# Kernel optimization log

Measured on AMD Instinct MI355X. Metric: run time of the kernel, lower is better.

## Reference

```python
import jax, jax.numpy as jnp
import numpy as np

B, N, F, D, DB, C = 1024, 200000, 32, 128, 256, 96


def _ln(x, g, b, eps=1e-5):
    m = x.mean(-1, keepdims=True)
    v = ((x - m) ** 2).mean(-1, keepdims=True)
    return (x - m) / jnp.sqrt(v + eps) * g + b


def setup_inputs() -> dict:
    key = jax.random.key(0)
    ks = jax.random.split(key, 24)
    s = 0.05
    inp = {
        'x_num': jax.random.normal(ks[0], (B, F), jnp.float32),
        'cand_x_num': jax.random.normal(ks[1], (N, F), jnp.float32),
        'cand_y': jax.random.normal(ks[2], (N,), jnp.float32),
        'W_in': jax.random.normal(ks[3], (F, D), jnp.float32) * s,
        'b_in': jnp.zeros((D,), jnp.float32),
        'enc_w1': jax.random.normal(ks[4], (D, DB), jnp.float32) * s,
        'enc_b1': jnp.zeros((DB,), jnp.float32),
        'enc_w2': jax.random.normal(ks[5], (DB, D), jnp.float32) * s,
        'enc_b2': jnp.zeros((D,), jnp.float32),
        'ln_mix_g': jnp.ones((D,), jnp.float32),
        'ln_mix_b': jnp.zeros((D,), jnp.float32),
        'K_w': jax.random.normal(ks[6], (D, D), jnp.float32) * s,
        'K_b': jnp.zeros((D,), jnp.float32),
        'lab_w': jax.random.normal(ks[7], (1, D), jnp.float32) * s,
        'lab_b': jnp.zeros((D,), jnp.float32),
        'T_w1': jax.random.normal(ks[8], (D, DB), jnp.float32) * s,
        'T_b1': jnp.zeros((DB,), jnp.float32),
        'T_w2': jax.random.normal(ks[9], (DB, D), jnp.float32) * s,  # no bias
        'pred_ln_g': jnp.ones((D,), jnp.float32),
        'pred_ln_b': jnp.zeros((D,), jnp.float32),
        'pred_w1': jax.random.normal(ks[10], (D, DB), jnp.float32) * s,
        'pred_b1': jnp.zeros((DB,), jnp.float32),
        'pred_w2': jax.random.normal(ks[11], (DB, D), jnp.float32) * s,
        'pred_b2': jnp.zeros((D,), jnp.float32),
        'head_ln_g': jnp.ones((D,), jnp.float32),
        'head_ln_b': jnp.zeros((D,), jnp.float32),
        'head_w': jax.random.normal(ks[12], (D, 1), jnp.float32) * s,
        'head_b': jnp.zeros((1,), jnp.float32),
        'context_size': C,
    }
    return inp


def _forward(x_num, cand_x_num, cand_y, W_in, b_in, enc_w1, enc_b1, enc_w2, enc_b2,
             ln_mix_g, ln_mix_b, K_w, K_b, lab_w, lab_b, T_w1, T_b1, T_w2,
             pred_ln_g, pred_ln_b, pred_w1, pred_b1, pred_w2, pred_b2,
             head_ln_g, head_ln_b, head_w, head_b, context_size):
    def enc(z):
        h = z @ W_in + b_in                                   # [*, D]
        h = h + (jax.nn.relu(h @ enc_w1 + enc_b1) @ enc_w2 + enc_b2)
        k = _ln(h, ln_mix_g, ln_mix_b) @ K_w + K_b
        return h, k

    cand_k = enc(cand_x_num)[1]                               # [N, D]
    x, k = enc(x_num)                                         # [B, D]

    # brute-force kNN: negative squared L2 via matmul + square sums
    k2 = (k * k).sum(-1, keepdims=True)                       # [B, 1]
    ck2 = (cand_k * cand_k).sum(-1)                           # [N]
    sims = 2.0 * (k @ cand_k.T) - k2 - ck2[None, :]           # [B, N]
    _, idx = jax.lax.top_k(sims, context_size)                # [B, C]

    context_k = cand_k[idx]                                   # [B, C, D]
    sim_c = 2.0 * jnp.einsum('bd,bcd->bc', k, context_k) - k2 - (context_k ** 2).sum(-1)
    probs = jax.nn.softmax(sim_c, axis=-1)                    # [B, C]

    ctx_y = cand_y[idx][..., None] @ lab_w + lab_b            # [B, C, D]
    diff = k[:, None, :] - context_k                          # [B, C, D]
    vals = ctx_y + jax.nn.relu(diff @ T_w1 + T_b1) @ T_w2     # [B, C, D]
    context_x = jnp.einsum('bc,bcd->bd', probs, vals)         # [B, D]

    x = x + context_x
    h = _ln(x, pred_ln_g, pred_ln_b)
    x = x + (jax.nn.relu(h @ pred_w1 + pred_b1) @ pred_w2 + pred_b2)
    out = jax.nn.relu(_ln(x, head_ln_g, head_ln_b)) @ head_w + head_b
    return out                                                # [B, 1]


def reference(x_num, cand_x_num, cand_y, W_in, b_in, enc_w1, enc_b1, enc_w2, enc_b2,
              ln_mix_g, ln_mix_b, K_w, K_b, lab_w, lab_b, T_w1, T_b1, T_w2,
              pred_ln_g, pred_ln_b, pred_w1, pred_b1, pred_w2, pred_b2,
              head_ln_g, head_ln_b, head_w, head_b, context_size):
    return _forward(x_num, cand_x_num, cand_y, W_in, b_in, enc_w1, enc_b1, enc_w2, enc_b2,
                    ln_mix_g, ln_mix_b, K_w, K_b, lab_w, lab_b, T_w1, T_b1, T_w2,
                    pred_ln_g, pred_ln_b, pred_w1, pred_b1, pred_w2, pred_b2,
                    head_ln_g, head_ln_b, head_w, head_b, context_size)
```

## Files before the change

### kernel.cpp

```cpp
#include <hip/hip_runtime.h>
#include <hip/hip_bf16.h>

#define NC 200000
#define NCP 200064
#define NCT 1563
#define NRG 196
#define CTR 8
#define SCAP2 32
#define CROW (NRG * SCAP2)
#define SREG 25
#define BB 1024
#define DD 128
#define DBH 256
#define CS 96

typedef __attribute__((ext_vector_type(8))) short bf16x8;
typedef __attribute__((ext_vector_type(4))) float f32x4;

#define LDH 136
#define LDU 264

__device__ inline uint4 pack8(const float4 a, const float4 b) {
  union { __hip_bfloat16 h[8]; uint4 v; } r;
  r.h[0] = __float2bfloat16(a.x); r.h[1] = __float2bfloat16(a.y);
  r.h[2] = __float2bfloat16(a.z); r.h[3] = __float2bfloat16(a.w);
  r.h[4] = __float2bfloat16(b.x); r.h[5] = __float2bfloat16(b.y);
  r.h[6] = __float2bfloat16(b.z); r.h[7] = __float2bfloat16(b.w);
  return r.v;
}

__device__ inline unsigned encf(float v) {
  unsigned b = __float_as_uint(v);
  return (b & 0x80000000u) ? ~b : (b | 0x80000000u);
}
__device__ inline float decf(unsigned u) {
  return __uint_as_float((u & 0x80000000u) ? (u ^ 0x80000000u) : ~u);
}
__device__ inline unsigned long long mkkey(float v, int idx) {
  unsigned u = encf(v);
  return (((unsigned long long)(~u)) << 32) | (unsigned)idx;
}

__device__ inline void gload16(const void* g, void* l) {
  __builtin_amdgcn_global_load_lds((const __attribute__((address_space(1))) void*)g,
                                   (__attribute__((address_space(3))) void*)l, 16, 0, 0);
}

__global__ __launch_bounds__(256) void k_prep(const float* __restrict__ w1,
                                              const float* __restrict__ w2,
                                              const float* __restrict__ kw,
                                              const float* __restrict__ tw1,
                                              __hip_bfloat16* __restrict__ w1t,
                                              __hip_bfloat16* __restrict__ w2t,
                                              __hip_bfloat16* __restrict__ kwt,
                                              __hip_bfloat16* __restrict__ tw1t) {
  const int i = blockIdx.x * 256 + threadIdx.x;
  if (i < 32768) {
    const int u = i >> 7, j = i & 127;
    w1t[i] = __float2bfloat16(w1[j * DBH + u]);
    tw1t[i] = __float2bfloat16(tw1[j * DBH + u]);
  }
  if (i < 32768) {
    const int d = i >> 8, u = i & 255;
    w2t[i] = __float2bfloat16(w2[u * DD + d]);
  }
  if (i < 16384) {
    const int d = i >> 7, j = i & 127;
    kwt[i] = __float2bfloat16(kw[j * DD + d]);
  }
}

__global__ __launch_bounds__(256) void k_pad(__hip_bfloat16* __restrict__ ckb16,
                                             float* __restrict__ ck2) {
  const int i = blockIdx.x * 256 + threadIdx.x;
  if (i < (NCP - NC) * DD) ckb16[(size_t)NC * DD + i] = __float2bfloat16(0.f);
  if (i < (NCP - NC)) ck2[NC + i] = 1e9f;
}

__global__ __launch_bounds__(256) void k_e1(const float* __restrict__ X,
                                            const float* __restrict__ W,
                                            const float* __restrict__ bias,
                                            float* __restrict__ H) {
  __shared__ float Xs[32 * 32];
  const int tid = threadIdx.x;
  const int r0 = blockIdx.x * 32;
  ((float4*)Xs)[tid] = ((const float4*)(X + (size_t)r0 * 32))[tid];
  __syncthreads();
  const int d0 = tid & 63;
  const int rh = tid >> 6;
  float acc0[8], acc1[8];
  const float b0 = bias[d0], b1 = bias[d0 + 64];
#pragma unroll
  for (int r = 0; r < 8; ++r) { acc0[r] = b0; acc1[r] = b1; }
#pragma unroll
  for (int k4 = 0; k4 < 8; ++k4) {
    float w0[4], w1[4];
#pragma unroll
    for (int kk = 0; kk < 4; ++kk) {
      w0[kk] = W[(k4 * 4 + kk) * DD + d0];
      w1[kk] = W[(k4 * 4 + kk) * DD + d0 + 64];
    }
#pragma unroll
    for (int r = 0; r < 8; ++r) {
      float4 x4 = ((const float4*)(Xs + (rh * 8 + r) * 32))[k4];
      acc0[r] += x4.x * w0[0] + x4.y * w0[1] + x4.z * w0[2] + x4.w * w0[3];
      acc1[r] += x4.x * w1[0] + x4.y * w1[1] + x4.z * w1[2] + x4.w * w1[3];
    }
  }
#pragma unroll
  for (int r = 0; r < 8; ++r) {
    const size_t row = (size_t)(r0 + rh * 8 + r);
    H[row * DD + d0] = acc0[r];
    H[row * DD + d0 + 64] = acc1[r];
  }
}

__global__ __launch_bounds__(256) void k_e23m(float* __restrict__ H,
                                              const __hip_bfloat16* __restrict__ W1t,
                                              const float* __restrict__ B1,
                                              const __hip_bfloat16* __restrict__ W2t,
                                              const float* __restrict__ B2) {
  __shared__ __hip_bfloat16 Hs[64 * LDH];
  __shared__ __hip_bfloat16 Us[64 * LDU];
  const int tid = threadIdx.x;
  const int r0 = blockIdx.x * 64;
#pragma unroll
  for (int i = 0; i < 4; ++i) {
    const int e8 = i * 256 + tid;
    const int row = e8 >> 4, c8 = e8 & 15;
    const float* src = H + (size_t)(r0 + row) * DD + c8 * 8;
    float4 f0 = *(const float4*)(src);
    float4 f1 = *(const float4*)(src + 4);
    *(uint4*)(Hs + row * LDH + c8 * 8) = pack8(f0, f1);
  }
  __syncthreads();
  const int l = tid & 63, w = tid >> 6;
  const int lr = l & 15, lg = l >> 4;
  {
    f32x4 acc[4][4] = {};
#pragma unroll
    for (int kk = 0; kk < 4; ++kk) {
      bf16x8 a[4], b[4];
#pragma unroll
      for (int mi = 0; mi < 4; ++mi)
        a[mi] = *(const bf16x8*)(Hs + (mi * 16 + lr) * LDH + kk * 32 + lg * 8);
#pragma unroll
      for (int ni = 0; ni < 4; ++ni)
        b[ni] = *(const bf16x8*)(W1t + (size_t)(w * 64 + ni * 16 + lr) * DD + kk * 32 + lg * 8);
#pragma unroll
      for (int mi = 0; mi < 4; ++mi)
#pragma unroll
        for (int ni = 0; ni < 4; ++ni)
          acc[mi][ni] = __builtin_amdgcn_mfma_f32_16x16x32_bf16(a[mi], b[ni], acc[mi][ni], 0, 0, 0);
    }
#pragma unroll
    for (int ni = 0; ni < 4; ++ni) {
      const int col = w * 64 + ni * 16 + lr;
      const float bb = B1[col];
#pragma unroll
      for (int mi = 0; mi < 4; ++mi)
#pragma unroll
        for (int r = 0; r < 4; ++r) {
          const int row = mi * 16 + lg * 4 + r;
          Us[row * LDU + col] = __float2bfloat16(fmaxf(acc[mi][ni][r] + bb, 0.f));
        }
    }
  }
  __syncthreads();
  {
    f32x4 acc[4][2] = {};
#pragma unroll
    for (int kk = 0; kk < 8; ++kk) {
      bf16x8 a[4], b[2];
#pragma unroll
      for (int mi = 0; mi < 4; ++mi)
        a[mi] = *(const bf16x8*)(Us + (mi * 16 + lr) * LDU + kk * 32 + lg * 8);
#pragma unroll
      for (int ni = 0; ni < 2; ++ni)
        b[ni] = *(const bf16x8*)(W2t + (size_t)(w * 32 + ni * 16 + lr) * DBH + kk * 32 + lg * 8);
#pragma unroll
      for (int mi = 0; mi < 4; ++mi)
#pragma unroll
        for (int ni = 0; ni < 2; ++ni)
          acc[mi][ni] = __builtin_amdgcn_mfma_f32_16x16x32_bf16(a[mi], b[ni], acc[mi][ni], 0, 0, 0);
    }
#pragma unroll
    for (int ni = 0; ni < 2; ++ni) {
      const int col = w * 32 + ni * 16 + lr;
      const float bb = B2[col];
#pragma unroll
      for (int mi = 0; mi < 4; ++mi)
#pragma unroll
        for (int r = 0; r < 4; ++r) {
          const int row = mi * 16 + lg * 4 + r;
          const size_t g = (size_t)(r0 + row) * DD + col;
          H[g] = H[g] + acc[mi][ni][r] + bb;
        }
    }
  }
}

__global__ __launch_bounds__(256) void k_e4m(const float* __restrict__ H,
                                             const float* __restrict__ g,
                                             const float* __restrict__ bln,
                                             const __hip_bfloat16* __restrict__ Kwt,
                                             const float* __restrict__ Kb,
                                             float* __restrict__ Kout,
                                             __hip_bfloat16* __restrict__ Kb16,
                                             float* __restrict__ k2out) {
  __shared__ __hip_bfloat16 Ls[64 * LDH];
  __shared__ float k2s[64];
  const int tid = threadIdx.x;
  const int r0 = blockIdx.x * 64;
  if (tid < 64) k2s[tid] = 0.f;
  {
    const int row = tid >> 2, q = tid & 3;
    const float* hr = H + (size_t)(r0 + row) * DD + q * 32;
    float v[32];
#pragma unroll
    for (int i = 0; i < 8; ++i) {
      float4 f = ((const float4*)hr)[i];
      v[i * 4 + 0] = f.x; v[i * 4 + 1] = f.y; v[i * 4 + 2] = f.z; v[i * 4 + 3] = f.w;
    }
    float s = 0.f;
#pragma unroll
    for (int i = 0; i < 32; ++i) s += v[i];
    s += __shfl_xor(s, 1); s += __shfl_xor(s, 2);
    const float mean = s * (1.f / 128.f);
    float vs = 0.f;
#pragma unroll
    for (int i = 0; i < 32; ++i) { float d = v[i] - mean; vs += d * d; }
    vs += __shfl_xor(vs, 1); vs += __shfl_xor(vs, 2);
    const float rstd = 1.f / sqrtf(vs * (1.f / 128.f) + 1e-5f);
#pragma unroll
    for (int i = 0; i < 4; ++i) {
      float t[8];
#pragma unroll
      for (int j = 0; j < 8; ++j) {
        const int col = q * 32 + i * 8 + j;
        t[j] = (v[i * 8 + j] - mean) * rstd * g[col] + bln[col];
      }
      float4 f0 = {t[0], t[1], t[2], t[3]}, f1 = {t[4], t[5], t[6], t[7]};
      *(uint4*)(Ls + row * LDH + q * 32 + i * 8) = pack8(f0, f1);
    }
  }
  __syncthreads();
  const int l = tid & 63, w = tid >> 6;
  const int lr = l & 15, lg = l >> 4;
  f32x4 acc[4][2] = {};
#pragma unroll
  for (int kk = 0; kk < 4; ++kk) {
    bf16x8 a[4], b[2];
#pragma unroll
    for (int mi = 0; mi < 4; ++mi)
      a[mi] = *(const bf16x8*)(Ls + (mi * 16 + lr) * LDH + kk * 32 + lg * 8);
#pragma unroll
    for (int ni = 0; ni < 2; ++ni)
      b[ni] = *(const bf16x8*)(Kwt + (size_t)(w * 32 + ni * 16 + lr) * DD + kk * 32 + lg * 8);
#pragma unroll
    for (int mi = 0; mi < 4; ++mi)
#pragma unroll
      for (int ni = 0; ni < 2; ++ni)
        acc[mi][ni] = __builtin_amdgcn_mfma_f32_16x16x32_bf16(a[mi], b[ni], acc[mi][ni], 0, 0, 0);
  }
  float p[4][4];
#pragma unroll
  for (int mi = 0; mi < 4; ++mi)
#pragma unroll
    for (int r = 0; r < 4; ++r) p[mi][r] = 0.f;
#pragma unroll
  for (int ni = 0; ni < 2; ++ni) {
    const int col = w * 32 + ni * 16 + lr;
    const float kb = Kb[col];
#pragma unroll
    for (int mi = 0; mi < 4; ++mi)
#pragma unroll
      for (int r = 0; r < 4; ++r) {
        const float val = acc[mi][ni][r] + kb;
        const int row = mi * 16 + lg * 4 + r;
        const size_t gg = (size_t)(r0 + row) * DD + col;
        Kout[gg] = val;
        Kb16[gg] = __float2bfloat16(val);
        p[mi][r] += val * val;
      }
  }
#pragma unroll
  for (int mi = 0; mi < 4; ++mi)
#pragma unroll
    for (int r = 0; r < 4; ++r) {
      float t = p[mi][r];
      t += __shfl_xor(t, 1); t += __shfl_xor(t, 2);
      t += __shfl_xor(t, 4); t += __shfl_xor(t, 8);
      if (lr == 0) atomicAdd(&k2s[mi * 16 + lg * 4 + r], t);
    }
  __syncthreads();
  if (tid < 64) k2out[r0 + tid] = k2s[tid];
}

__global__ __launch_bounds__(256) void k_simsA(const __hip_bfloat16* __restrict__ A,
                                               const __hip_bfloat16* __restrict__ Bm,
                                               const float* __restrict__ ck2,
                                               float* __restrict__ rmaxpart) {
  __shared__ __hip_bfloat16 Bs[128 * 128];
  __shared__ float part[2][128];
  const int tid = threadIdx.x;
  const int bid = blockIdx.x;
  const int gq = bid >> 6, rt = (bid >> 3) & 7, xq = bid & 7;
  const int range = gq * 8 + xq;
  if (range >= NRG) return;
  const int m0 = rt * 128;
  const int l = tid & 63, w = tid >> 6;
  const int wm = w >> 1, wn = w & 1;
  const int lr = l & 15, lg = l >> 4;
  bf16x8 a[4][4];
#pragma unroll
  for (int mi = 0; mi < 4; ++mi) {
    const __hip_bfloat16* ar = A + (size_t)(m0 + wm * 64 + mi * 16 + lr) * DD + lg * 8;
#pragma unroll
    for (int kk = 0; kk < 4; ++kk) a[mi][kk] = *(const bf16x8*)(ar + kk * 32);
  }
  float vmax[4][4];
#pragma unroll
  for (int mi = 0; mi < 4; ++mi)
#pragma unroll
    for (int r = 0; r < 4; ++r) vmax[mi][r] = -1e30f;
  for (int i = 0; i < CTR; ++i) {
    const int ct = range * CTR + i;
    if (ct >= NCT) break;
    const int n0 = ct * 128;
    {
      const char* gbase = (const char*)(Bm + (size_t)n0 * DD);
#pragma unroll
      for (int j = 0; j < 8; ++j) {
        const int r = w * 32 + j * 4 + (l >> 4);
        const int b = ((l & 15) * 16) ^ ((r & 7) << 4);
        gload16(gbase + (size_t)r * 256 + b, (char*)Bs + w * 8192 + j * 1024);
      }
    }
    float c2l[4];
#pragma unroll
    for (int ni = 0; ni < 4; ++ni) c2l[ni] = 0.5f * ck2[n0 + wn * 64 + ni * 16 + lr];
    __syncthreads();
    f32x4 acc[4][4] = {};
#pragma unroll
    for (int kk = 0; kk < 4; ++kk) {
      bf16x8 b[4];
#pragma unroll
      for (int ni = 0; ni < 4; ++ni) {
        const int row = wn * 64 + ni * 16 + lr;
        const int boff = (kk * 64 + lg * 16) ^ ((row & 7) << 4);
        b[ni] = *(const bf16x8*)((const char*)Bs + row * 256 + boff);
      }
#pragma unroll
      for (int mi = 0; mi < 4; ++mi)
#pragma unroll
        for (int ni = 0; ni < 4; ++ni)
          acc[mi][ni] = __builtin_amdgcn_mfma_f32_16x16x32_bf16(a[mi][kk], b[ni], acc[mi][ni], 0, 0, 0);
    }
#pragma unroll
    for (int mi = 0; mi < 4; ++mi)
#pragma unroll
      for (int r = 0; r < 4; ++r)
#pragma unroll
        for (int ni = 0; ni < 4; ++ni)
          vmax[mi][r] = fmaxf(vmax[mi][r], acc[mi][ni][r] - c2l[ni]);
    __syncthreads();
  }
#pragma unroll
  for (int mi = 0; mi < 4; ++mi)
#pragma unroll
    for (int r = 0; r < 4; ++r) {
      float v = vmax[mi][r];
#pragma unroll
      for (int mk = 1; mk < 16; mk <<= 1) v = fmaxf(v, __shfl_xor(v, mk));
      if (lr == 0) part[wn][wm * 64 + mi * 16 + lg * 4 + r] = v;
    }
  __syncthreads();
  if (tid < 128)
    rmaxpart[(size_t)range * BB + m0 + tid] = fmaxf(part[0][tid], part[1][tid]);
}

__global__ __launch_bounds__(256) void k_rmax(const float* __restrict__ rmaxpart,
                                              float* __restrict__ cutF) {
  const int row = blockIdx.x * 256 + threadIdx.x;
  float m = -1e30f;
  for (int j = 0; j < NRG; ++j) m = fmaxf(m, rmaxpart[(size_t)j * BB + row]);
  const float t = m - 7.0f;
  cutF[row] = t - (fabsf(t) + 8.0f) * 0.00390625f - 1e-5f;
}

__global__ __launch_bounds__(256) void k_simsB(const __hip_bfloat16* __restrict__ A,
                                               const __hip_bfloat16* __restrict__ Bm,
                                               const float* __restrict__ ck2,
                                               const float* __restrict__ cutF,
                                               unsigned long long* __restrict__ cand,
                                               int* __restrict__ cnt2) {
  __shared__ __hip_bfloat16 Bs[128 * 128];
  __shared__ float cut_s[128];
  __shared__ int lcnt[128];
  const int tid = threadIdx.x;
  const int bid = blockIdx.x;
  const int gq = bid >> 6, rt = (bid >> 3) & 7, xq = bid & 7;
  const int range = gq * 8 + xq;
  if (range >= NRG) return;
  const int m0 = rt * 128;
  if (tid < 128) { cut_s[tid] = cutF[m0 + tid]; lcnt[tid] = 0; }
  const int l = tid & 63, w = tid >> 6;
  const int wm = w >> 1, wn = w & 1;
  const int lr = l & 15, lg = l >> 4;
  bf16x8 a[4][4];
#pragma unroll
  for (int mi = 0; mi < 4; ++mi) {
    const __hip_bfloat16* ar = A + (size_t)(m0 + wm * 64 + mi * 16 + lr) * DD + lg * 8;
#pragma unroll
    for (int kk = 0; kk < 4; ++kk) a[mi][kk] = *(const bf16x8*)(ar + kk * 32);
  }
  for (int i = 0; i < CTR; ++i) {
    const int ct = range * CTR + i;
    if (ct >= NCT) break;
    const int n0 = ct * 128;
    {
      const char* gbase = (const char*)(Bm + (size_t)n0 * DD);
#pragma unroll
      for (int j = 0; j < 8; ++j) {
        const int r = w * 32 + j * 4 + (l >> 4);
        const int b = ((l & 15) * 16) ^ ((r & 7) << 4);
        gload16(gbase + (size_t)r * 256 + b, (char*)Bs + w * 8192 + j * 1024);
      }
    }
    float c2l[4];
#pragma unroll
    for (int ni = 0; ni < 4; ++ni) c2l[ni] = 0.5f * ck2[n0 + wn * 64 + ni * 16 + lr];
    __syncthreads();
    f32x4 acc[4][4] = {};
#pragma unroll
    for (int kk = 0; kk < 4; ++kk) {
      bf16x8 b[4];
#pragma unroll
      for (int ni = 0; ni < 4; ++ni) {
        const int row = wn * 64 + ni * 16 + lr;
        const int boff = (kk * 64 + lg * 16) ^ ((row & 7) << 4);
        b[ni] = *(const bf16x8*)((const char*)Bs + row * 256 + boff);
      }
#pragma unroll
      for (int mi = 0; mi < 4; ++mi)
#pragma unroll
        for (int ni = 0; ni < 4; ++ni)
          acc[mi][ni] = __builtin_amdgcn_mfma_f32_16x16x32_bf16(a[mi][kk], b[ni], acc[mi][ni], 0, 0, 0);
    }
#pragma unroll
    for (int ni = 0; ni < 4; ++ni) {
      const int gcol = n0 + wn * 64 + ni * 16 + lr;
#pragma unroll
      for (int mi = 0; mi < 4; ++mi)
#pragma unroll
        for (int r = 0; r < 4; ++r) {
          const int lrow = wm * 64 + mi * 16 + lg * 4 + r;
          const float x = acc[mi][ni][r] - c2l[ni];
          if (x >= cut_s[lrow]) {
            const float v = __bfloat162float(__float2bfloat16(x));
            const int q = atomicAdd(&lcnt[lrow], 1);
            if (q < SCAP2)
              cand[(size_t)(m0 + lrow) * CROW + range * SCAP2 + q] = mkkey(v, gcol);
          }
        }
    }
    __syncthreads();
  }
  if (tid < 128) {
    const int n = lcnt[tid];
    cnt2[(size_t)range * BB + m0 + tid] = n < SCAP2 ? n : SCAP2;
  }
}

__global__ __launch_bounds__(256) void k_sortB(const unsigned long long* __restrict__ cand,
                                               const int* __restrict__ cnt2,
                                               int* __restrict__ idx_out) {
  __shared__ unsigned long long keys[CROW];
  __shared__ int csum[NRG + 1];
  __shared__ int wred[40][4];
  __shared__ int outl[128];
  __shared__ int outc_sh;
  const int tid = threadIdx.x;
  const int wid = tid >> 6, lane = tid & 63;
  const int row = blockIdx.x;
  if (tid < NRG) csum[tid] = cnt2[(size_t)tid * BB + row];
  __syncthreads();
  if (tid == 0) {
    int s = 0;
    for (int j = 0; j < NRG; ++j) { const int c = csum[j]; csum[j] = s; s += c; }
    csum[NRG] = s;
  }
  __syncthreads();
  const int n = csum[NRG];
  if (tid < NRG) {
    const int base = csum[tid], c = csum[tid + 1] - base;
    const unsigned long long* src = cand + (size_t)row * CROW + tid * SCAP2;
    for (int j = 0; j < c; ++j) keys[base + j] = src[j];
  }
  __syncthreads();

  unsigned v16l[SREG];
  int idl[SREG];
#pragma unroll
  for (int s = 0; s < SREG; ++s) {
    const int i = tid + s * 256;
    if (i < n) {
      const unsigned long long k = keys[i];
      v16l[s] = (~(unsigned)(k >> 32)) >> 16;
      idl[s] = (int)(k & 0xFFFFFFFFu);
    } else {
      v16l[s] = 0u;
      idl[s] = 0x7FFFFFFF;
    }
  }

  int pass = 0;
  unsigned prefix = 0;
  int need = CS;
#pragma unroll
  for (int b = 15; b >= 0; --b) {
    int c1 = 0;
#pragma unroll
    for (int s = 0; s < SREG; ++s)
      c1 += ((v16l[s] >> (b + 1)) == prefix && ((v16l[s] >> b) & 1u)) ? 1 : 0;
#pragma unroll
    for (int d = 1; d < 64; d <<= 1) c1 += __shfl_xor(c1, d);
    if (lane == 0) wred[pass][wid] = c1;
    __syncthreads();
    const int cnt1 = wred[pass][0] + wred[pass][1] + wred[pass][2] + wred[pass][3];
    ++pass;
    if (need <= cnt1) prefix = (prefix << 1) | 1u;
    else { need -= cnt1; prefix = (prefix << 1); }
  }
  const unsigned V16star = prefix;

  unsigned iprefix = 0;
  int ineed = need;
#pragma unroll
  for (int b = 17; b >= 0; --b) {
    int c0 = 0;
#pragma unroll
    for (int s = 0; s < SREG; ++s)
      c0 += (v16l[s] == V16star && ((unsigned)idl[s] >> (b + 1)) == iprefix &&
             !(((unsigned)idl[s] >> b) & 1u)) ? 1 : 0;
#pragma unroll
    for (int d = 1; d < 64; d <<= 1) c0 += __shfl_xor(c0, d);
    if (lane == 0) wred[pass][wid] = c0;
    __syncthreads();
    const int cnt0 = wred[pass][0] + wred[pass][1] + wred[pass][2] + wred[pass][3];
    ++pass;
    if (ineed <= cnt0) iprefix = (iprefix << 1);
    else { ineed -= cnt0; iprefix = (iprefix << 1) | 1u; }
  }
  const unsigned ITstar = iprefix;

  if (tid == 0) outc_sh = 0;
  __syncthreads();
#pragma unroll
  for (int s = 0; s < SREG; ++s) {
    if (v16l[s] > V16star || (v16l[s] == V16star && (unsigned)idl[s] <= ITstar)) {
      const int q = atomicAdd(&outc_sh, 1);
      if (q < 128) outl[q] = idl[s];
    }
  }
  __syncthreads();
  const int ne = outc_sh;
  for (int i = tid; i < 128; i += 256)
    if (i >= ne) outl[i] = 0x7FFFFFFF;
  __syncthreads();
  for (int k = 2; k <= 128; k <<= 1) {
    for (int j = k >> 1; j > 0; j >>= 1) {
      if (tid < 128) {
        const int i = tid, ixj = i ^ j;
        if (ixj > i) {
          int a = outl[i], b = outl[ixj];
          const bool up = ((i & k) == 0);
          if ((a > b) == up) { outl[i] = b; outl[ixj] = a; }
        }
      }
      __syncthreads();
    }
  }
  if (tid < CS) {
    int id = outl[tid];
    if ((unsigned)id >= NC) id = 0;
    idx_out[row * CS + tid] = id;
  }
}

#define LDB 136
__global__ __launch_bounds__(256) void k_final(const float* __restrict__ XH,
                                               const float* __restrict__ XK,
                                               const float* __restrict__ CK,
                                               const float* __restrict__ CY,
                                               const int* __restrict__ IDX,
                                               const __hip_bfloat16* __restrict__ Tw1t,
                                               const float* __restrict__ Tb1,
                                               const float* __restrict__ Tw2,
                                               const float* __restrict__ labw,
                                               const float* __restrict__ labb,
                                               const float* __restrict__ pg,
                                               const float* __restrict__ pb,
                                               const float* __restrict__ pw1,
                                               const float* __restrict__ pb1,
                                               const float* __restrict__ pw2,
                                               const float* __restrict__ pb2,
                                               const float* __restrict__ hg,
                                               const float* __restrict__ hb,
                                               const float* __restrict__ hw,
                                               const float* __restrict__ hbias,
                                               float* __restrict__ OUT) {
  __shared__ float diffs[CS * 132];
  __shared__ int ids[CS];
  __shared__ float yv[CS], simc[CS], pr[CS];
  __shared__ float kv[DD], xv[DD];
  __shared__ float qs[DBH];
  __shared__ float xrow[DD], hln[DD], t2[DBH], x2[DD];
  __shared__ float red[DD];
  __shared__ float smv[1];
  const int tid = threadIdx.x;
  const int b = blockIdx.x;
  if (tid < CS) ids[tid] = IDX[b * CS + tid];
  if (tid < DD) { kv[tid] = XK[(size_t)b * DD + tid]; xv[tid] = XH[(size_t)b * DD + tid]; }
  __syncthreads();
  if (tid < CS) yv[tid] = CY[ids[tid]];
  for (int e = tid; e < CS * DD; e += 256) {
    const int c = e >> 7, j = e & 127;
    diffs[c * 132 + j] = kv[j] - CK[(size_t)ids[c] * DD + j];
  }
  __syncthreads();
  if (tid < CS) {
    float s = 0.f;
    for (int j = 0; j < DD; ++j) { float d = diffs[tid * 132 + j]; s -= d * d; }
    simc[tid] = s;
  }
  __syncthreads();
  if (tid < DD) red[tid] = (tid < CS) ? simc[tid] : -1e30f;
  __syncthreads();
  for (int s = 64; s > 0; s >>= 1) { if (tid < s) red[tid] = fmaxf(red[tid], red[tid + s]); __syncthreads(); }
  const float mx = red[0];
  __syncthreads();
  if (tid < DD) red[tid] = (tid < CS) ? expf(simc[tid] - mx) : 0.f;
  if (tid < CS) pr[tid] = expf(simc[tid] - mx);
  __syncthreads();
  for (int s = 64; s > 0; s >>= 1) { if (tid < s) red[tid] += red[tid + s]; __syncthreads(); }
  const float inv = 1.f / red[0];
  __syncthreads();
  if (tid < CS) pr[tid] *= inv;
  if (tid < DD) red[tid] = (tid < CS) ? pr[tid] * yv[tid] : 0.f;
  __syncthreads();
  for (int s = 64; s > 0; s >>= 1) { if (tid < s) red[tid] += red[tid + s]; __syncthreads(); }
  if (tid == 0) smv[0] = red[0];
  __hip_bfloat16* db16 = (__hip_bfloat16*)diffs;
  {
    float4 f0s[6], f1s[6];
#pragma unroll
    for (int i = 0; i < 6; ++i) {
      const int gidx = tid + 256 * i;
      const int row = gidx >> 4, c8 = gidx & 15;
      f0s[i] = *(const float4*)(diffs + row * 132 + c8 * 8);
      f1s[i] = *(const float4*)(diffs + row * 132 + c8 * 8 + 4);
    }
    __syncthreads();
#pragma unroll
    for (int i = 0; i < 6; ++i) {
      const int gidx = tid + 256 * i;
      const int row = gidx >> 4, c8 = gidx & 15;
      *(uint4*)(db16 + row * LDB + c8 * 8) = pack8(f0s[i], f1s[i]);
    }
  }
  __syncthreads();
  {
    const int w = tid >> 6, l = tid & 63;
    const int lr = l & 15, lg = l >> 4;
    const int u0 = w * 64;
    bf16x8 af[6][4];
#pragma unroll
    for (int mt = 0; mt < 6; ++mt)
#pragma unroll
      for (int k = 0; k < 4; ++k)
        af[mt][k] = *(const bf16x8*)(db16 + (mt * 16 + lr) * LDB + k * 32 + lg * 8);
#pragma unroll
    for (int nt = 0; nt < 4; ++nt) {
      const int u = u0 + nt * 16 + lr;
      bf16x8 bfr[4];
#pragma unroll
      for (int k = 0; k < 4; ++k)
        bfr[k] = *(const bf16x8*)(Tw1t + (size_t)u * DD + k * 32 + lg * 8);
      const float bb = Tb1[u];
      float qacc = 0.f;
#pragma unroll
      for (int mt = 0; mt < 6; ++mt) {
        f32x4 acc = {};
#pragma unroll
        for (int k = 0; k < 4; ++k)
          acc = __builtin_amdgcn_mfma_f32_16x16x32_bf16(af[mt][k], bfr[k], acc, 0, 0, 0);
#pragma unroll
        for (int r = 0; r < 4; ++r) {
          const int c = mt * 16 + lg * 4 + r;
          qacc += pr[c] * fmaxf(acc[r] + bb, 0.f);
        }
      }
      qacc += __shfl_xor(qacc, 16);
      qacc += __shfl_xor(qacc, 32);
      if (lg == 0) qs[u] = qacc;
    }
  }
  __syncthreads();
  if (tid < DD) {
    const int d = tid;
    float cx = smv[0] * labw[d] + labb[d];
    for (int u4 = 0; u4 < 64; ++u4) {
      float4 q4 = *(const float4*)(&qs[u4 * 4]);
      cx += q4.x * Tw2[(u4 * 4 + 0) * DD + d];
      cx += q4.y * Tw2[(u4 * 4 + 1) * DD + d];
      cx += q4.z * Tw2[(u4 * 4 + 2) * DD + d];
      cx += q4.w * Tw2[(u4 * 4 + 3) * DD + d];
    }
    xrow[d] = xv[d] + cx;
  }
  __syncthreads();
  if (tid < DD) red[tid] = xrow[tid];
  __syncthreads();
  for (int s = 64; s > 0; s >>= 1) { if (tid < s) red[tid] += red[tid + s]; __syncthreads(); }
  const float m1 = red[0] * (1.f / 128.f);
  __syncthreads();
  if (tid < DD) { float d = xrow[tid] - m1; red[tid] = d * d; }
  __syncthreads();
  for (int s = 64; s > 0; s >>= 1) { if (tid < s) red[tid] += red[tid + s]; __syncthreads(); }
  const float rstd1 = 1.f / sqrtf(red[0] * (1.f / 128.f) + 1e-5f);
  __syncthreads();
  if (tid < DD) hln[tid] = (xrow[tid] - m1) * rstd1 * pg[tid] + pb[tid];
  __syncthreads();
  {
    const int u = tid;
    float s = pb1[u];
    for (int j4 = 0; j4 < 32; ++j4) {
      float4 h4 = *(const float4*)(hln + j4 * 4);
      s += h4.x * pw1[(j4 * 4 + 0) * DBH + u];
      s += h4.y * pw1[(j4 * 4 + 1) * DBH + u];
      s += h4.z * pw1[(j4 * 4 + 2) * DBH + u];
      s += h4.w * pw1[(j4 * 4 + 3) * DBH + u];
    }
    t2[u] = fmaxf(s, 0.f);
  }
  __syncthreads();
  if (tid < DD) {
    const int d = tid;
    float s = pb2[d];
    for (int u4 = 0; u4 < 64; ++u4) {
      float4 t4 = *(const float4*)(t2 + u4 * 4);
      s += t4.x * pw2[(u4 * 4 + 0) * DD + d];
      s += t4.y * pw2[(u4 * 4 + 1) * DD + d];
      s += t4.z * pw2[(u4 * 4 + 2) * DD + d];
      s += t4.w * pw2[(u4 * 4 + 3) * DD + d];
    }
    x2[d] = xrow[d] + s;
  }
  __syncthreads();
  if (tid < DD) red[tid] = x2[tid];
  __syncthreads();
  for (int s = 64; s > 0; s >>= 1) { if (tid < s) red[tid] += red[tid + s]; __syncthreads(); }
  const float m2 = red[0] * (1.f / 128.f);
  __syncthreads();
  if (tid < DD) { float d = x2[tid] - m2; red[tid] = d * d; }
  __syncthreads();
  for (int s = 64; s > 0; s >>= 1) { if (tid < s) red[tid] += red[tid + s]; __syncthreads(); }
  const float rstd2 = 1.f / sqrtf(red[0] * (1.f / 128.f) + 1e-5f);
  __syncthreads();
  if (tid < DD) {
    float z = (x2[tid] - m2) * rstd2 * hg[tid] + hb[tid];
    z = fmaxf(z, 0.f);
    red[tid] = z * hw[tid];
  }
  __syncthreads();
  for (int s = 64; s > 0; s >>= 1) { if (tid < s) red[tid] += red[tid + s]; __syncthreads(); }
  if (tid == 0) OUT[b] = red[0] + hbias[0];
}

extern "C" void kernel_launch(void* const* d_in, const int* in_sizes, int n_in,
                              void* d_out, int out_size, void* d_ws, size_t ws_size,
                              hipStream_t stream) {
  (void)in_sizes; (void)n_in; (void)out_size; (void)ws_size;
  const float* x_num      = (const float*)d_in[0];
  const float* cand_x     = (const float*)d_in[1];
  const float* cand_y     = (const float*)d_in[2];
  const float* W_in       = (const float*)d_in[3];
  const float* b_in       = (const float*)d_in[4];
  const float* enc_w1     = (const float*)d_in[5];
  const float* enc_b1     = (const float*)d_in[6];
  const float* enc_w2     = (const float*)d_in[7];
  const float* enc_b2     = (const float*)d_in[8];
  const float* ln_mix_g   = (const float*)d_in[9];
  const float* ln_mix_b   = (const float*)d_in[10];
  const float* K_w        = (const float*)d_in[11];
  const float* K_b        = (const float*)d_in[12];
  const float* lab_w      = (const float*)d_in[13];
  const float* lab_b      = (const float*)d_in[14];
  const float* T_w1       = (const float*)d_in[15];
  const float* T_b1       = (const float*)d_in[16];
  const float* T_w2       = (const float*)d_in[17];
  const float* pred_ln_g  = (const float*)d_in[18];
  const float* pred_ln_b  = (const float*)d_in[19];
  const float* pred_w1    = (const float*)d_in[20];
  const float* pred_b1    = (const float*)d_in[21];
  const float* pred_w2    = (const float*)d_in[22];
  const float* pred_b2    = (const float*)d_in[23];
  const float* head_ln_g  = (const float*)d_in[24];
  const float* head_ln_b  = (const float*)d_in[25];
  const float* head_w     = (const float*)d_in[26];
  const float* head_b     = (const float*)d_in[27];
  float* out = (float*)d_out;

  char* w8 = (char*)d_ws;
  size_t off = 0;
  float* cand_k = (float*)(w8 + off);              off += (size_t)NC * DD * 4;
  float* cand_ck2 = (float*)(w8 + off);            off += (size_t)NCP * 4 + 256;
  float* xh = (float*)(w8 + off);                  off += (size_t)BB * DD * 4;
  float* xk = (float*)(w8 + off);                  off += (size_t)BB * DD * 4;
  float* xk2 = (float*)(w8 + off);                 off += 4096;
  __hip_bfloat16* xkb16 = (__hip_bfloat16*)(w8 + off); off += (size_t)BB * DD * 2;
  int* idx_all = (int*)(w8 + off);                 off += (size_t)BB * CS * 4;
  __hip_bfloat16* w1t = (__hip_bfloat16*)(w8 + off); off += (size_t)DBH * DD * 2;
  __hip_bfloat16* w2t = (__hip_bfloat16*)(w8 + off); off += (size_t)DD * DBH * 2;
  __hip_bfloat16* kwt = (__hip_bfloat16*)(w8 + off); off += (size_t)DD * DD * 2;
  __hip_bfloat16* tw1t = (__hip_bfloat16*)(w8 + off); off += (size_t)DBH * DD * 2;
  char* big = w8 + off;
  float* cand_h = (float*)big;
  unsigned long long* candb = (unsigned long long*)big;
  float* rmaxpart = (float*)(big + (size_t)56 * 1024 * 1024);
  int* cnt2 = (int*)(big + (size_t)57 * 1024 * 1024);
  float* cutF = (float*)(big + (size_t)58 * 1024 * 1024);
  __hip_bfloat16* ckb16 = (__hip_bfloat16*)(big + (size_t)NC * DD * 4);

  k_prep<<<128, 256, 0, stream>>>(enc_w1, enc_w2, K_w, T_w1, w1t, w2t, kwt, tw1t);
  k_pad<<<32, 256, 0, stream>>>(ckb16, cand_ck2);
  k_e1<<<NC / 32, 256, 0, stream>>>(cand_x, W_in, b_in, cand_h);
  k_e23m<<<NC / 64, 256, 0, stream>>>(cand_h, w1t, enc_b1, w2t, enc_b2);
  k_e4m<<<NC / 64, 256, 0, stream>>>(cand_h, ln_mix_g, ln_mix_b, kwt, K_b,
                                     cand_k, ckb16, cand_ck2);
  k_e1<<<BB / 32, 256, 0, stream>>>(x_num, W_in, b_in, xh);
  k_e23m<<<BB / 64, 256, 0, stream>>>(xh, w1t, enc_b1, w2t, enc_b2);
  k_e4m<<<BB / 64, 256, 0, stream>>>(xh, ln_mix_g, ln_mix_b, kwt, K_b,
                                     xk, xkb16, xk2);
  k_simsA<<<1600, 256, 0, stream>>>(xkb16, ckb16, cand_ck2, rmaxpart);
  k_rmax<<<4, 256, 0, stream>>>(rmaxpart, cutF);
  k_simsB<<<1600, 256, 0, stream>>>(xkb16, ckb16, cand_ck2, cutF, candb, cnt2);
  k_sortB<<<BB, 256, 0, stream>>>(candb, cnt2, idx_all);
  k_final<<<BB, 256, 0, stream>>>(xh, xk, cand_k, cand_y, idx_all,
                                  tw1t, T_b1, T_w2, lab_w, lab_b,
                                  pred_ln_g, pred_ln_b, pred_w1, pred_b1, pred_w2, pred_b2,
                                  head_ln_g, head_ln_b, head_w, head_b, out);
}
```

Before: 582.2 us.

## Double-buffer candidate tiles in LDS for similarity kernels

Both similarity kernels (simsA and simsB) now use two LDS buffers for the candidate-key tile and issue the async global-to-LDS load of the next tile before computing the current one. This aims to overlap global memory latency with MFMA work and drops one barrier per iteration. In exchange, LDS use per block doubles to about 64KB, which may reduce occupancy. There is also a possible race: the prefetch relies on the single barrier at the end of each iteration, and the async load may not have completed when the barrier is reached, since there is no explicit vmcnt wait.

Measured after the change: 574.7 us. No clear change (-1.3%).

```diff
diff --git a/kernel.cpp b/kernel.cpp
--- a/kernel.cpp
+++ b/kernel.cpp
@@ -44,6 +44,17 @@
 __device__ inline void gload16(const void* g, void* l) {
   __builtin_amdgcn_global_load_lds((const __attribute__((address_space(1))) void*)g,
                                    (__attribute__((address_space(3))) void*)l, 16, 0, 0);
+}
+
+__device__ inline void stageB(const __hip_bfloat16* __restrict__ Bm, int n0,
+                              __hip_bfloat16* buf, int w, int l) {
+  const char* gbase = (const char*)(Bm + (size_t)n0 * DD);
+#pragma unroll
+  for (int j = 0; j < 8; ++j) {
+    const int r = w * 32 + j * 4 + (l >> 4);
+    const int b = ((l & 15) * 16) ^ ((r & 7) << 4);
+    gload16(gbase + (size_t)r * 256 + b, (char*)buf + w * 8192 + j * 1024);
+  }
 }
 
 __global__ __launch_bounds__(256) void k_prep(const float* __restrict__ w1,
@@ -301,7 +312,7 @@
                                                const __hip_bfloat16* __restrict__ Bm,
                                                const float* __restrict__ ck2,
                                                float* __restrict__ rmaxpart) {
-  __shared__ __hip_bfloat16 Bs[128 * 128];
+  __shared__ __hip_bfloat16 Bs[2][128 * 128];
   __shared__ float part[2][128];
   const int tid = threadIdx.x;
   const int bid = blockIdx.x;
@@ -312,6 +323,8 @@
   const int l = tid & 63, w = tid >> 6;
   const int wm = w >> 1, wn = w & 1;
   const int lr = l & 15, lg = l >> 4;
+  const int ct0 = range * CTR;
+  const int nt = (ct0 + CTR <= NCT) ? CTR : (NCT - ct0);
   bf16x8 a[4][4];
 #pragma unroll
   for (int mi = 0; mi < 4; ++mi) {
@@ -324,23 +337,15 @@
   for (int mi = 0; mi < 4; ++mi)
 #pragma unroll
     for (int r = 0; r < 4; ++r) vmax[mi][r] = -1e30f;
-  for (int i = 0; i < CTR; ++i) {
-    const int ct = range * CTR + i;
-    if (ct >= NCT) break;
-    const int n0 = ct * 128;
-    {
-      const char* gbase = (const char*)(Bm + (size_t)n0 * DD);
-#pragma unroll
-      for (int j = 0; j < 8; ++j) {
-        const int r = w * 32 + j * 4 + (l >> 4);
-        const int b = ((l & 15) * 16) ^ ((r & 7) << 4);
-        gload16(gbase + (size_t)r * 256 + b, (char*)Bs + w * 8192 + j * 1024);
-      }
-    }
+  stageB(Bm, ct0 * 128, Bs[0], w, l);
+  __syncthreads();
+  int cur = 0;
+  for (int i = 0; i < nt; ++i) {
+    const int n0 = (ct0 + i) * 128;
     float c2l[4];
 #pragma unroll
     for (int ni = 0; ni < 4; ++ni) c2l[ni] = 0.5f * ck2[n0 + wn * 64 + ni * 16 + lr];
-    __syncthreads();
+    if (i + 1 < nt) stageB(Bm, n0 + 128, Bs[cur ^ 1], w, l);
     f32x4 acc[4][4] = {};
 #pragma unroll
     for (int kk = 0; kk < 4; ++kk) {
@@ -349,7 +354,7 @@
       for (int ni = 0; ni < 4; ++ni) {
         const int row = wn * 64 + ni * 16 + lr;
         const int boff = (kk * 64 + lg * 16) ^ ((row & 7) << 4);
-        b[ni] = *(const bf16x8*)((const char*)Bs + row * 256 + boff);
+        b[ni] = *(const bf16x8*)((const char*)Bs[cur] + row * 256 + boff);
       }
 #pragma unroll
       for (int mi = 0; mi < 4; ++mi)
@@ -365,6 +370,7 @@
         for (int ni = 0; ni < 4; ++ni)
           vmax[mi][r] = fmaxf(vmax[mi][r], acc[mi][ni][r] - c2l[ni]);
     __syncthreads();
+    cur ^= 1;
   }
 #pragma unroll
   for (int mi = 0; mi < 4; ++mi)
@@ -395,7 +401,7 @@
                                                const float* __restrict__ cutF,
                                                unsigned long long* __restrict__ cand,
                                                int* __restrict__ cnt2) {
-  __shared__ __hip_bfloat16 Bs[128 * 128];
+  __shared__ __hip_bfloat16 Bs[2][128 * 128];
   __shared__ float cut_s[128];
   __shared__ int lcnt[128];
   const int tid = threadIdx.x;
@@ -408,6 +414,8 @@
   const int l = tid & 63, w = tid >> 6;
   const int wm = w >> 1, wn = w & 1;
   const int lr = l & 15, lg = l >> 4;
+  const int ct0 = range * CTR;
+  const int nt = (ct0 + CTR <= NCT) ? CTR : (NCT - ct0);
   bf16x8 a[4][4];
 #pragma unroll
   for (int mi = 0; mi < 4; ++mi) {
@@ -415,23 +423,15 @@
 #pragma unroll
     for (int kk = 0; kk < 4; ++kk) a[mi][kk] = *(const bf16x8*)(ar + kk * 32);
   }
-  for (int i = 0; i < CTR; ++i) {
-    const int ct = range * CTR + i;
-    if (ct >= NCT) break;
-    const int n0 = ct * 128;
-    {
-      const char* gbase = (const char*)(Bm + (size_t)n0 * DD);
-#pragma unroll
-      for (int j = 0; j < 8; ++j) {
-        const int r = w * 32 + j * 4 + (l >> 4);
-        const int b = ((l & 15) * 16) ^ ((r & 7) << 4);
-        gload16(gbase + (size_t)r * 256 + b, (char*)Bs + w * 8192 + j * 1024);
-      }
-    }
+  stageB(Bm, ct0 * 128, Bs[0], w, l);
+  __syncthreads();
+  int cur = 0;
+  for (int i = 0; i < nt; ++i) {
+    const int n0 = (ct0 + i) * 128;
     float c2l[4];
 #pragma unroll
     for (int ni = 0; ni < 4; ++ni) c2l[ni] = 0.5f * ck2[n0 + wn * 64 + ni * 16 + lr];
-    __syncthreads();
+    if (i + 1 < nt) stageB(Bm, n0 + 128, Bs[cur ^ 1], w, l);
     f32x4 acc[4][4] = {};
 #pragma unroll
     for (int kk = 0; kk < 4; ++kk) {
@@ -440,7 +440,7 @@
       for (int ni = 0; ni < 4; ++ni) {
         const int row = wn * 64 + ni * 16 + lr;
         const int boff = (kk * 64 + lg * 16) ^ ((row & 7) << 4);
-        b[ni] = *(const bf16x8*)((const char*)Bs + row * 256 + boff);
+        b[ni] = *(const bf16x8*)((const char*)Bs[cur] + row * 256 + boff);
       }
 #pragma unroll
       for (int mi = 0; mi < 4; ++mi)
@@ -466,6 +466,7 @@
         }
     }
     __syncthreads();
+    cur ^= 1;
   }
   if (tid < 128) {
     const int n = lcnt[tid];
```
